# Performance work log

Hardware: AMD Instinct MI355X
Metric: run time of the kernel (lower is better)

The kernel has to match this reference:

```python
import jax, jax.numpy as jnp
import numpy as np

N, L, I, H, D = 8192, 8, 256, 512, 8
PER = N // D  # nodes per depth level; level 0 nodes are tree roots


def setup_inputs() -> dict:
    key = jax.random.key(0)
    ks = jax.random.split(key, 9)
    s = 0.05
    x_seq = jax.random.normal(ks[0], (N, L, I), jnp.float32)
    # GRU params (torch nn.GRU layout, gate order r,z,n), stored transposed [in, 3H]
    W_ih = jax.random.normal(ks[1], (I, 3 * H), jnp.float32) * s
    W_hh = jax.random.normal(ks[2], (H, 3 * H), jnp.float32) * s
    b_ih = jax.random.normal(ks[3], (3 * H,), jnp.float32) * s
    b_hh = jax.random.normal(ks[4], (3 * H,), jnp.float32) * s
    # Child-sum TreeLSTM params: x-projections for i,o,u,f and recurrent U's
    Wx = jax.random.normal(ks[5], (H, 4 * H), jnp.float32) * s
    bx = jax.random.normal(ks[6], (4 * H,), jnp.float32) * s
    U_iou = jax.random.normal(ks[7], (H, 3 * H), jnp.float32) * s
    U_f = jax.random.normal(ks[8], (H, H), jnp.float32) * s
    # Forest structure: D levels of PER nodes; node at level d>0 has a random
    # parent at level d-1; roots (level 0) point at themselves (contribution is
    # zero because their own state is still zero when level 0 is processed).
    rng = np.random.default_rng(0)
    depth = np.repeat(np.arange(D), PER).astype(np.int32)
    parent = np.arange(N, dtype=np.int32)
    for d in range(1, D):
        parent[d * PER:(d + 1) * PER] = rng.integers((d - 1) * PER, d * PER, PER)
    root_ids = np.arange(PER, dtype=np.int32)
    return {
        "x_seq": x_seq, "W_ih": W_ih, "W_hh": W_hh, "b_ih": b_ih, "b_hh": b_hh,
        "Wx": Wx, "bx": bx, "U_iou": U_iou, "U_f": U_f,
        "parent": jnp.asarray(parent), "depth": jnp.asarray(depth),
        "root_ids": jnp.asarray(root_ids), "n_levels": D,
    }


def reference(x_seq, W_ih, W_hh, b_ih, b_hh, Wx, bx, U_iou, U_f,
              parent, depth, root_ids, n_levels):
    n = x_seq.shape[0]
    h_dim = W_hh.shape[0]

    # --- GRU over each node's encoding sequence (all nodes batched) ---
    def gru_step(h, x_t):  # h: [N,H], x_t: [N,I]
        gi = x_t @ W_ih + b_ih
        gh = h @ W_hh + b_hh
        ir, iz, inn = jnp.split(gi, 3, axis=-1)
        hr, hz, hn = jnp.split(gh, 3, axis=-1)
        r = jax.nn.sigmoid(ir + hr)
        z = jax.nn.sigmoid(iz + hz)
        ng = jnp.tanh(inn + r * hn)
        return (1.0 - z) * ng + z * h, None

    h0 = jnp.zeros((n, h_dim), x_seq.dtype)
    enc, _ = jax.lax.scan(gru_step, h0, jnp.swapaxes(x_seq, 0, 1))  # [N,H]

    # --- Child-sum TreeLSTM, processed leaves -> roots by depth level ---
    xg = enc @ Wx + bx  # [N,4H]
    xi, xo, xu, xf = jnp.split(xg, 4, axis=-1)
    c = jnp.zeros((n, h_dim), x_seq.dtype)
    h = jnp.zeros((n, h_dim), x_seq.dtype)
    for level in range(n_levels - 1, -1, -1):
        h_sum = jax.ops.segment_sum(h, parent, num_segments=n)  # sum over children
        giou = h_sum @ U_iou
        i = jax.nn.sigmoid(xi + giou[:, :h_dim])
        o = jax.nn.sigmoid(xo + giou[:, h_dim:2 * h_dim])
        u = jnp.tanh(xu + giou[:, 2 * h_dim:])
        # per-child forget gate uses parent's x projection and child's h
        f = jax.nn.sigmoid(xf[parent] + h @ U_f)
        fc = jax.ops.segment_sum(f * c, parent, num_segments=n)
        c_new = i * u + fc
        mask = (depth == level)[:, None]
        c = jnp.where(mask, c_new, c)
        h = jnp.where(mask, o * jnp.tanh(c_new), h)

    # root states per tree, stacked as [2, n_trees, H] -> (c_root, h_root)
    return jnp.stack([c[root_ids], h[root_ids]])
```

## Files before the change

### kernel.cpp

```cpp
#include <hip/hip_runtime.h>
#include <math.h>

typedef short bf16x8 __attribute__((ext_vector_type(8)));
typedef float f32x4 __attribute__((ext_vector_type(4)));

__device__ __forceinline__ float sigf(float x) {
    return __builtin_amdgcn_rcpf(1.f + __expf(-x));
}
__device__ __forceinline__ float tanhf_fast(float x) {
    const float e = __expf(2.f * x);
    return 1.f - 2.f * __builtin_amdgcn_rcpf(e + 1.f);
}

__device__ __forceinline__ unsigned short f2bf(float f) {
    union { float f; unsigned u; } v; v.f = f;
    unsigned r = (v.u + 0x7FFFu + ((v.u >> 16) & 1u)) >> 16;
    return (unsigned short)r;
}
__device__ __forceinline__ float bf2f(unsigned short u) {
    union { unsigned u; float f; } v; v.u = ((unsigned)u) << 16; return v.f;
}

__device__ __forceinline__ void gload16(const unsigned short* g, unsigned short* l) {
    __builtin_amdgcn_global_load_lds(
        (const __attribute__((address_space(1))) void*)g,
        (__attribute__((address_space(3))) void*)l, 16, 0, 0);
}

__device__ __forceinline__ int swz(int slot, int row) {
    return (slot ^ ((row >> 1) & 3)) * 8;
}
__device__ __forceinline__ int tix(int ml, int jl) {
    return ((ml >> 4) * 2 + (jl >> 5)) * 512 + (ml & 15) * 32 + (jl & 31);
}

__global__ void cvt_f32_bf16(const float* __restrict__ src,
                             unsigned short* __restrict__ dst, int n)
{
    const int i = (blockIdx.x * blockDim.x + threadIdx.x) * 4;
    if (i >= n) return;
    const float4 v = *reinterpret_cast<const float4*>(src + i);
    ushort4 o;
    o.x = f2bf(v.x); o.y = f2bf(v.y); o.z = f2bf(v.z); o.w = f2bf(v.w);
    *reinterpret_cast<ushort4*>(dst + i) = o;
}

__global__ void transpose_cvt(const float* __restrict__ src,
                              unsigned short* __restrict__ dst,
                              int rows, int cols)
{
    __shared__ float tile[32][33];
    const int bc = blockIdx.x * 32, br = blockIdx.y * 32;
    const int tx = threadIdx.x, ty = threadIdx.y;
    #pragma unroll
    for (int i = 0; i < 32; i += 8)
        tile[ty + i][tx] = src[(size_t)(br + ty + i) * cols + bc + tx];
    __syncthreads();
    #pragma unroll
    for (int i = 0; i < 32; i += 8)
        dst[(size_t)(bc + ty + i) * rows + br + tx] = f2bf(tile[tx][ty + i]);
}

__global__ __launch_bounds__(256)
void gemm_bf16out(const unsigned short* __restrict__ A,
                  const unsigned short* __restrict__ BT,
                  const float* __restrict__ bias,
                  unsigned short* __restrict__ Cb, int M, int N, int K,
                  int ncols, int Mrows, int rstride, int tstride)
{
    const int nwg = (int)gridDim.x;
    const int l = ((int)blockIdx.x & 7) * (nwg >> 3) + ((int)blockIdx.x >> 3);
    const int m0 = (l / ncols) * 128, n0 = (l % ncols) * 128;
    const size_t abase = (size_t)(m0 % Mrows) * rstride
                       + (size_t)(m0 / Mrows) * tstride;
    const int tid = (int)threadIdx.x, lane = tid & 63, wid = tid >> 6;
    const int wm = wid >> 1, wn = wid & 1;
    const int fr = lane & 15, kg = lane >> 4;
    const int lrow = lane >> 2;
    const int scol = swz(lane & 3, lrow);

    __shared__ unsigned short smem[3 * 8192];

    f32x4 acc[4][4];
    #pragma unroll
    for (int i = 0; i < 4; ++i)
        #pragma unroll
        for (int j = 0; j < 4; ++j)
            acc[i][j] = (f32x4){0.f, 0.f, 0.f, 0.f};

    auto stage = [&](int buf, int kt) {
        const int k0 = kt * 32;
        unsigned short* base = &smem[buf * 8192];
        #pragma unroll
        for (int q = 0; q < 4; ++q) {
            const int c = wid * 4 + q;
            const unsigned short* g = (c < 8)
                ? A + abase + (size_t)(c * 16 + lrow) * rstride + k0 + scol
                : BT + (size_t)(n0 + (c - 8) * 16 + lrow) * K + k0 + scol;
            gload16(g, base + c * 512);
        }
    };

    const int nkt = K >> 5;
    stage(0, 0); stage(1, 1); stage(2, 2);
    int cur = 0;

    for (int kt = 0; kt < nkt; ++kt) {
        if (kt + 2 < nkt)      asm volatile("s_waitcnt vmcnt(8)" ::: "memory");
        else if (kt + 1 < nkt) asm volatile("s_waitcnt vmcnt(4)" ::: "memory");
        else                   asm volatile("s_waitcnt vmcnt(0)" ::: "memory");
        __builtin_amdgcn_s_barrier();

        const unsigned short* sb = &smem[cur * 8192];
        bf16x8 af[4], bf[4];
        #pragma unroll
        for (int mi = 0; mi < 4; ++mi) {
            const int row = wm * 64 + mi * 16 + fr;
            af[mi] = *reinterpret_cast<const bf16x8*>(&sb[row * 32 + swz(kg, row)]);
        }
        #pragma unroll
        for (int ni = 0; ni < 4; ++ni) {
            const int row = wn * 64 + ni * 16 + fr;
            bf[ni] = *reinterpret_cast<const bf16x8*>(&sb[4096 + row * 32 + swz(kg, row)]);
        }
        asm volatile("s_waitcnt lgkmcnt(0)" ::: "memory");
        __builtin_amdgcn_s_barrier();
        if (kt + 3 < nkt) stage(cur, kt + 3);

        __builtin_amdgcn_s_setprio(1);
        #pragma unroll
        for (int mi = 0; mi < 4; ++mi)
            #pragma unroll
            for (int ni = 0; ni < 4; ++ni)
                acc[mi][ni] = __builtin_amdgcn_mfma_f32_16x16x32_bf16(
                    af[mi], bf[ni], acc[mi][ni], 0, 0, 0);
        __builtin_amdgcn_s_setprio(0);
        cur = (cur == 2) ? 0 : cur + 1;
    }

    #pragma unroll
    for (int ni = 0; ni < 4; ++ni) {
        const int nl = wn * 64 + ni * 16 + fr;
        const float bv = bias[n0 + nl];
        #pragma unroll
        for (int mi = 0; mi < 4; ++mi)
            #pragma unroll
            for (int r = 0; r < 4; ++r) {
                const int ml = wm * 64 + mi * 16 + kg * 4 + r;
                smem[ml * 132 + nl] = f2bf(acc[mi][ni][r] + bv);
            }
    }
    __syncthreads();
    #pragma unroll
    for (int e = 0; e < 8; ++e) {
        const int id = tid + e * 256;
        const int row = id >> 4, cw = id & 15;
        const int4 v = *reinterpret_cast<const int4*>(&smem[row * 132 + cw * 8]);
        *reinterpret_cast<int4*>(&Cb[(size_t)(m0 + row) * N + n0 + cw * 8]) = v;
    }
}

__global__ void gru_step0(const unsigned short* __restrict__ gi,
                          unsigned short* __restrict__ hbo,
                          const float* __restrict__ b_hh)
{
    constexpr int H = 512, G3H = 1536;
    const int idx = blockIdx.x * blockDim.x + threadIdx.x;
    const int m = idx >> 6, jv = idx & 63;
    const size_t gb = (size_t)m * G3H + jv * 8;
    const bf16x8 gr8 = *reinterpret_cast<const bf16x8*>(gi + gb);
    const bf16x8 gz8 = *reinterpret_cast<const bf16x8*>(gi + gb + H);
    const bf16x8 gn8 = *reinterpret_cast<const bf16x8*>(gi + gb + 2 * H);
    bf16x8 o;
    #pragma unroll
    for (int k = 0; k < 8; ++k) {
        const int j = jv * 8 + k;
        const float r = sigf(bf2f((unsigned short)gr8[k]) + b_hh[j]);
        const float z = sigf(bf2f((unsigned short)gz8[k]) + b_hh[H + j]);
        const float n = tanhf_fast(bf2f((unsigned short)gn8[k]) + r * b_hh[2 * H + j]);
        o[k] = (short)f2bf((1.f - z) * n);
    }
    *reinterpret_cast<bf16x8*>(hbo + (size_t)m * H + jv * 8) = o;
}

__global__ __launch_bounds__(256, 3)
void gru_step(const unsigned short* __restrict__ giT,
              const unsigned short* __restrict__ hbi,
              unsigned short* __restrict__ hbo,
              const unsigned short* __restrict__ WhhT,
              const float* __restrict__ b_hh)
{
    constexpr int H = 512, G3H = 1536;
    const int m0 = blockIdx.x * 64, j0 = blockIdx.y * 64;
    const int tid = (int)threadIdx.x, lane = tid & 63, wid = tid >> 6;
    const int wm = wid >> 1, wn = wid & 1;
    const int fr = lane & 15, kg = lane >> 4;
    const int lrow = lane >> 2;
    const int scol = swz(lane & 3, lrow);
    const int ucol = (lane & 3) * 8;

    __shared__ unsigned short smem[3 * 8192];

    f32x4 ar[2][2], az[2][2], ah[2][2];
    #pragma unroll
    for (int i = 0; i < 2; ++i)
        #pragma unroll
        for (int j = 0; j < 2; ++j) {
            ar[i][j] = (f32x4){0.f, 0.f, 0.f, 0.f};
            az[i][j] = (f32x4){0.f, 0.f, 0.f, 0.f};
            ah[i][j] = (f32x4){0.f, 0.f, 0.f, 0.f};
        }

    constexpr int nkt = H / 32;

    auto stage = [&](int buf, int kt) {
        const int k0 = kt * 32;
        unsigned short* base = &smem[buf * 8192];
        #pragma unroll
        for (int q = 0; q < 4; ++q) {
            const int c = wid * 4 + q;
            if (c < 4) {
                const unsigned short* g =
                    hbi + (size_t)(m0 + c * 16 + lrow) * H + k0 + scol;
                gload16(g, base + c * 512);
            } else {
                const int gate = (c - 4) >> 2, rowg = (c - 4) & 3;
                const unsigned short* g =
                    WhhT + (size_t)(gate * H + j0 + rowg * 16 + lrow) * H + k0 + scol;
                gload16(g, base + c * 512);
            }
        }
    };
    auto stage_epi = [&](int ep) {
        unsigned short* base = &smem[(ep + 1) * 8192];
        #pragma unroll
        for (int q = 0; q < 4; ++q) {
            const int c = wid * 4 + q;
            const int part = c >> 3, cc = c & 7;
            const int rowg = cc >> 1, colg = cc & 1;
            const unsigned short* src;
            if (ep == 0)
                src = giT + (size_t)(m0 + rowg * 16 + lrow) * G3H
                          + part * H + j0 + colg * 32 + ucol;
            else if (part == 0)
                src = giT + (size_t)(m0 + rowg * 16 + lrow) * G3H
                          + 2 * H + j0 + colg * 32 + ucol;
            else
                src = hbi + (size_t)(m0 + rowg * 16 + lrow) * H
                          + j0 + colg * 32 + ucol;
            gload16(src, base + part * 4096 + cc * 512);
        }
    };

    stage(0, 0); stage(1, 1); stage(2, 2);
    int cur = 0;

    for (int kt = 0; kt < nkt; ++kt) {
        asm volatile("s_waitcnt vmcnt(8)" ::: "memory");
        __builtin_amdgcn_s_barrier();

        const unsigned short* sb = &smem[cur * 8192];
        bf16x8 af[2], bfr[2], bfz[2], bfn[2];
        #pragma unroll
        for (int mi = 0; mi < 2; ++mi) {
            const int row = wm * 32 + mi * 16 + fr;
            af[mi] = *reinterpret_cast<const bf16x8*>(&sb[row * 32 + swz(kg, row)]);
        }
        #pragma unroll
        for (int ni = 0; ni < 2; ++ni) {
            const int row = wn * 32 + ni * 16 + fr;
            const int sw = swz(kg, row);
            bfr[ni] = *reinterpret_cast<const bf16x8*>(&sb[2048 + (row) * 32 + sw]);
            bfz[ni] = *reinterpret_cast<const bf16x8*>(&sb[2048 + (64 + row) * 32 + sw]);
            bfn[ni] = *reinterpret_cast<const bf16x8*>(&sb[2048 + (128 + row) * 32 + sw]);
        }
        asm volatile("s_waitcnt lgkmcnt(0)" ::: "memory");
        __builtin_amdgcn_s_barrier();
        if (kt + 3 < nkt)       stage(cur, kt + 3);
        else if (kt == nkt - 3) stage_epi(0);
        else if (kt == nkt - 2) stage_epi(1);

        __builtin_amdgcn_s_setprio(1);
        #pragma unroll
        for (int mi = 0; mi < 2; ++mi)
            #pragma unroll
            for (int ni = 0; ni < 2; ++ni) {
                ar[mi][ni] = __builtin_amdgcn_mfma_f32_16x16x32_bf16(af[mi], bfr[ni], ar[mi][ni], 0, 0, 0);
                az[mi][ni] = __builtin_amdgcn_mfma_f32_16x16x32_bf16(af[mi], bfz[ni], az[mi][ni], 0, 0, 0);
                ah[mi][ni] = __builtin_amdgcn_mfma_f32_16x16x32_bf16(af[mi], bfn[ni], ah[mi][ni], 0, 0, 0);
            }
        __builtin_amdgcn_s_setprio(0);
        cur = (cur == 2) ? 0 : cur + 1;
    }

    asm volatile("s_waitcnt vmcnt(0)" ::: "memory");
    __builtin_amdgcn_s_barrier();

    unsigned short res[2][2][4];
    #pragma unroll
    for (int ni = 0; ni < 2; ++ni) {
        const int jl = wn * 32 + ni * 16 + fr;
        const int j = j0 + jl;
        const float bhr = b_hh[j], bhz = b_hh[H + j], bhn = b_hh[2 * H + j];
        #pragma unroll
        for (int mi = 0; mi < 2; ++mi) {
            #pragma unroll
            for (int r = 0; r < 4; ++r) {
                const int ml = wm * 32 + mi * 16 + kg * 4 + r;
                const int ix = tix(ml, jl);
                const float gr = bf2f(smem[8192 + ix]);
                const float gz = bf2f(smem[12288 + ix]);
                const float gn = bf2f(smem[16384 + ix]);
                const float hv = bf2f(smem[20480 + ix]);
                const float rg = sigf(ar[mi][ni][r] + gr + bhr);
                const float zg = sigf(az[mi][ni][r] + gz + bhz);
                const float ng = tanhf_fast(gn + rg * (ah[mi][ni][r] + bhn));
                res[ni][mi][r] = f2bf((1.f - zg) * ng + zg * hv);
            }
        }
    }

    #pragma unroll
    for (int ni = 0; ni < 2; ++ni) {
        const int jl = wn * 32 + ni * 16 + fr;
        #pragma unroll
        for (int mi = 0; mi < 2; ++mi)
            #pragma unroll
            for (int r = 0; r < 4; ++r) {
                const int ml = wm * 32 + mi * 16 + kg * 4 + r;
                smem[tix(ml, jl)] = res[ni][mi][r];
            }
    }
    __syncthreads();

    #pragma unroll
    for (int e = 0; e < 2; ++e) {
        const int id = tid + e * 256;
        const int ml = id >> 3, jw = id & 7;
        const int4 v = *reinterpret_cast<const int4*>(
            &smem[((ml >> 4) * 2 + (jw >> 2)) * 512 + (ml & 15) * 32 + (jw & 3) * 8]);
        *reinterpret_cast<int4*>(&hbo[(size_t)(m0 + ml) * H + j0 + jw * 8]) = v;
    }
}

__global__ __launch_bounds__(256, 4)
void tree_gemm(const unsigned short* __restrict__ hTb,
               const unsigned short* __restrict__ UcombT,
               const unsigned short* __restrict__ xgb,
               const float* __restrict__ cT,
               const int* __restrict__ parent,
               int cstart, int pstart,
               float* __restrict__ giou,
               float* __restrict__ fcs)
{
    constexpr int H = 512, N4H = 2048, G3H = 1536;
    const int nwg = (int)gridDim.x;
    const int l = ((int)blockIdx.x & 7) * (nwg >> 3) + ((int)blockIdx.x >> 3);
    const int m0 = (l >> 5) * 64, n0 = (l & 31) * 64;
    const int tid = (int)threadIdx.x, lane = tid & 63, wid = tid >> 6;
    const int wm = wid >> 1, wn = wid & 1;
    const int fr = lane & 15, kg = lane >> 4;
    const int lrow = lane >> 2;
    const int scol = swz(lane & 3, lrow);

    __shared__ unsigned short smem[4 * 4096];

    f32x4 acc[2][2];
    #pragma unroll
    for (int i = 0; i < 2; ++i)
        #pragma unroll
        for (int j = 0; j < 2; ++j)
            acc[i][j] = (f32x4){0.f, 0.f, 0.f, 0.f};

    auto stage = [&](int buf, int kt) {
        const int k0 = kt * 32;
        unsigned short* base = &smem[buf * 4096];
        #pragma unroll
        for (int q = 0; q < 2; ++q) {
            const int c = wid * 2 + q;
            const unsigned short* g = (c < 4)
                ? hTb + (size_t)(cstart + m0 + c * 16 + lrow) * H + k0 + scol
                : UcombT + (size_t)(n0 + (c - 4) * 16 + lrow) * H + k0 + scol;
            gload16(g, base + c * 512);
        }
    };

    constexpr int nkt = H / 32;
    stage(0, 0); stage(1, 1); stage(2, 2); stage(3, 3);
    int cur = 0;

    for (int kt = 0; kt < nkt; ++kt) {
        if (kt + 3 < nkt)      asm volatile("s_waitcnt vmcnt(6)" ::: "memory");
        else if (kt + 2 < nkt) asm volatile("s_waitcnt vmcnt(4)" ::: "memory");
        else if (kt + 1 < nkt) asm volatile("s_waitcnt vmcnt(2)" ::: "memory");
        else                   asm volatile("s_waitcnt vmcnt(0)" ::: "memory");
        __builtin_amdgcn_s_barrier();

        const unsigned short* sb = &smem[cur * 4096];
        bf16x8 af[2], bf[2];
        #pragma unroll
        for (int mi = 0; mi < 2; ++mi) {
            const int row = wm * 32 + mi * 16 + fr;
            af[mi] = *reinterpret_cast<const bf16x8*>(&sb[row * 32 + swz(kg, row)]);
        }
        #pragma unroll
        for (int ni = 0; ni < 2; ++ni) {
            const int row = wn * 32 + ni * 16 + fr;
            bf[ni] = *reinterpret_cast<const bf16x8*>(&sb[2048 + row * 32 + swz(kg, row)]);
        }
        asm volatile("s_waitcnt lgkmcnt(0)" ::: "memory");
        __builtin_amdgcn_s_barrier();
        if (kt + 4 < nkt) stage(cur, kt + 4);

        __builtin_amdgcn_s_setprio(1);
        #pragma unroll
        for (int mi = 0; mi < 2; ++mi)
            #pragma unroll
            for (int ni = 0; ni < 2; ++ni)
                acc[mi][ni] = __builtin_amdgcn_mfma_f32_16x16x32_bf16(
                    af[mi], bf[ni], acc[mi][ni], 0, 0, 0);
        __builtin_amdgcn_s_setprio(0);
        cur = (cur == 3) ? 0 : cur + 1;
    }

    if (n0 < G3H) {
        #pragma unroll
        for (int mi = 0; mi < 2; ++mi)
            #pragma unroll
            for (int r = 0; r < 4; ++r) {
                const int m = m0 + wm * 32 + mi * 16 + kg * 4 + r;
                const int p = parent[cstart + m] - pstart;
                #pragma unroll
                for (int ni = 0; ni < 2; ++ni) {
                    const int n = n0 + wn * 32 + ni * 16 + fr;
                    atomicAdd(&giou[(size_t)p * G3H + n], acc[mi][ni][r]);
                }
            }
    } else {
        #pragma unroll
        for (int mi = 0; mi < 2; ++mi)
            #pragma unroll
            for (int r = 0; r < 4; ++r) {
                const int m = m0 + wm * 32 + mi * 16 + kg * 4 + r;
                const int child = cstart + m;
                const int p = parent[child];
                #pragma unroll
                for (int ni = 0; ni < 2; ++ni) {
                    const int jf = n0 + wn * 32 + ni * 16 + fr - G3H;
                    const float f = sigf(acc[mi][ni][r] +
                                         bf2f(xgb[(size_t)p * N4H + G3H + jf]));
                    atomicAdd(&fcs[(size_t)(p - pstart) * H + jf],
                              f * cT[(size_t)child * H + jf]);
                }
            }
    }
}

__global__ void level_update(const unsigned short* __restrict__ xgb,
                             float* __restrict__ giou,
                             float* __restrict__ fcs,
                             float* __restrict__ cT, float* __restrict__ hT,
                             unsigned short* __restrict__ hb, int pstart,
                             float* __restrict__ outp, int PH)
{
    constexpr int H = 512, N4H = 2048, G3H = 1536;
    const int idx = blockIdx.x * blockDim.x + threadIdx.x;
    const int pi = idx >> 9, j = idx & (H - 1);
    const int p = pstart + pi;
    const size_t xb4 = (size_t)p * N4H;
    const size_t gb = (size_t)pi * G3H;
    const float ig = sigf(bf2f(xgb[xb4 + j]) + giou[gb + j]);
    const float og = sigf(bf2f(xgb[xb4 + H + j]) + giou[gb + H + j]);
    const float ug = tanhf_fast(bf2f(xgb[xb4 + 2 * H + j]) + giou[gb + 2 * H + j]);
    const float cn = ig * ug + fcs[idx];
    const float hn = og * tanhf_fast(cn);
    if (outp) {
        outp[idx] = cn;
        outp[(size_t)PH + idx] = hn;
    } else {
        const size_t off = (size_t)p * H + j;
        cT[off] = cn;
        hT[off] = hn;
        hb[off] = f2bf(hn);
        giou[gb + j] = 0.f;
        giou[gb + H + j] = 0.f;
        giou[gb + 2 * H + j] = 0.f;
        fcs[idx] = 0.f;
    }
}

extern "C" void kernel_launch(void* const* d_in, const int* in_sizes, int n_in,
                              void* d_out, int out_size, void* d_ws, size_t ws_size,
                              hipStream_t stream)
{
    const float* x_seq = (const float*)d_in[0];
    const float* W_ih  = (const float*)d_in[1];
    const float* W_hh  = (const float*)d_in[2];
    const float* b_ih  = (const float*)d_in[3];
    const float* b_hh  = (const float*)d_in[4];
    const float* Wx    = (const float*)d_in[5];
    const float* bx    = (const float*)d_in[6];
    const float* U_iou = (const float*)d_in[7];
    const float* U_f   = (const float*)d_in[8];
    const int* parent  = (const int*)d_in[9];

    const int threeH = in_sizes[3];
    const int H   = threeH / 3;
    const int I   = in_sizes[1] / threeH;
    const int N   = in_sizes[9];
    const int L   = in_sizes[0] / (N * I);
    const int PER = in_sizes[11];
    const int D   = N / PER;

    const size_t NH = (size_t)N * H;
    const size_t PH = (size_t)PER * H;
    const size_t NG = (size_t)N * threeH;

    char* p = (char*)d_ws;
    const size_t xb_sz  = (size_t)N * L * I * 2;
    const size_t xgb_sz = (size_t)N * 4 * H * 2;
    const size_t zone_sz = xb_sz > xgb_sz ? xb_sz : xgb_sz;
    unsigned short* xb  = (unsigned short*)p;
    unsigned short* xgb = (unsigned short*)p;    p += zone_sz;
    unsigned short* gi  = (unsigned short*)p;    p += (size_t)N * L * threeH * 2;
    unsigned short* hb0 = (unsigned short*)p;    p += NH * 2;
    unsigned short* hb1 = (unsigned short*)p;    p += NH * 2;
    unsigned short* WihT = (unsigned short*)p;   p += (size_t)threeH * I * 2;
    unsigned short* WhhT = (unsigned short*)p;   p += (size_t)threeH * H * 2;
    unsigned short* WxT  = (unsigned short*)p;   p += (size_t)4 * H * H * 2;
    unsigned short* UcombT = (unsigned short*)p; p += (size_t)4 * H * H * 2;
    if ((size_t)(p - (char*)d_ws) > ws_size) return;
    float* cT   = (float*)gi;
    float* hT   = cT + NH;
    float* giou = hT + NH;
    float* fcs  = giou + PH * 3;

    {
        const int n = N * L * I;
        cvt_f32_bf16<<<(n / 4 + 255) / 256, 256, 0, stream>>>(x_seq, xb, n);
        dim3 blk(32, 8);
        transpose_cvt<<<dim3(threeH / 32, I / 32), blk, 0, stream>>>(W_ih, WihT, I, threeH);
        transpose_cvt<<<dim3(threeH / 32, H / 32), blk, 0, stream>>>(W_hh, WhhT, H, threeH);
        transpose_cvt<<<dim3(4 * H / 32, H / 32), blk, 0, stream>>>(Wx, WxT, H, 4 * H);
        transpose_cvt<<<dim3(threeH / 32, H / 32), blk, 0, stream>>>(U_iou, UcombT, H, threeH);
        transpose_cvt<<<dim3(H / 32, H / 32), blk, 0, stream>>>(
            U_f, UcombT + (size_t)threeH * H, H, H);
    }

    gemm_bf16out<<<(N * L / 128) * (threeH / 128), 256, 0, stream>>>(
        xb, WihT, b_ih, gi, N * L, threeH, I, threeH / 128,
        N, L * I, I);

    gru_step0<<<(int)(NH / 8 / 256), 256, 0, stream>>>(gi, hb1, b_hh);
    {
        dim3 grid(N / 64, H / 64);
        for (int t = 1; t < L; ++t) {
            const unsigned short* hin = (t & 1) ? hb1 : hb0;
            unsigned short* hout = (t & 1) ? hb0 : hb1;
            gru_step<<<grid, 256, 0, stream>>>(gi + (size_t)t * NG, hin, hout,
                                               WhhT, b_hh);
        }
    }

    gemm_bf16out<<<(N / 128) * (4 * H / 128), 256, 0, stream>>>(
        hb0, WxT, bx, xgb, N, 4 * H, H, 4 * H / 128,
        N, H, 0);

    hipMemsetAsync(giou, 0, PH * 4 * 4, stream);
    unsigned short* hTb = hb1;
    const int pw_blocks = (int)(PH / 256);

    for (int lvl = D - 1; lvl >= 0; --lvl) {
        const int pstart = lvl * PER;
        const int cstart = (lvl + 1) * PER;

        if (lvl < D - 1)
            tree_gemm<<<(PER / 64) * (4 * H / 64), 256, 0, stream>>>(
                hTb, UcombT, xgb, cT, parent, cstart, pstart, giou, fcs);

        level_update<<<pw_blocks, 256, 0, stream>>>(
            xgb, giou, fcs, cT, hT, hTb, pstart,
            (lvl == 0) ? (float*)d_out : nullptr, (int)PH);
    }
}
```

Measured before the change: 471.8 us.

## Double-buffer GRU step for higher occupancy and merge setup launches

The GRU recurrent step kernel drops from triple to double buffering in LDS and raises launch bounds from 3 to 4 blocks per CU, aiming for higher occupancy. The epilogue operands now reuse the two buffers, which requires an extra barrier. The five weight-transpose launches are folded into one kernel that picks its source by block index. The memset of the tree accumulators is replaced by a priming flag on the first level_update, which skips reading them and always zeroes them. The cost is a shallower prefetch pipeline in the GRU step, which may expose more memory latency.

```diff
diff --git a/kernel.cpp b/kernel.cpp
--- a/kernel.cpp
+++ b/kernel.cpp
@@ -45,12 +45,28 @@
     *reinterpret_cast<ushort4*>(dst + i) = o;
 }
 
-__global__ void transpose_cvt(const float* __restrict__ src,
-                              unsigned short* __restrict__ dst,
-                              int rows, int cols)
-{
+__global__ void transpose_all(const float* __restrict__ W_ih,
+                              const float* __restrict__ W_hh,
+                              const float* __restrict__ Wx,
+                              const float* __restrict__ U_iou,
+                              const float* __restrict__ U_f,
+                              unsigned short* __restrict__ WihT,
+                              unsigned short* __restrict__ WhhT,
+                              unsigned short* __restrict__ WxT,
+                              unsigned short* __restrict__ UcombT,
+                              int threeH, int I, int H,
+                              int n1, int n2, int n3, int n4)
+{
+    int b = (int)blockIdx.x;
+    const float* src; unsigned short* dst; int rows, cols;
+    if (b < n1)      { src = W_ih;  dst = WihT;   rows = I; cols = threeH; }
+    else if (b < n2) { src = W_hh;  dst = WhhT;   rows = H; cols = threeH; b -= n1; }
+    else if (b < n3) { src = Wx;    dst = WxT;    rows = H; cols = 4 * H;  b -= n2; }
+    else if (b < n4) { src = U_iou; dst = UcombT; rows = H; cols = threeH; b -= n3; }
+    else { src = U_f; dst = UcombT + (size_t)threeH * H; rows = H; cols = H; b -= n4; }
+    const int ncx = cols / 32;
+    const int bc = (b % ncx) * 32, br = (b / ncx) * 32;
     __shared__ float tile[32][33];
-    const int bc = blockIdx.x * 32, br = blockIdx.y * 32;
     const int tx = threadIdx.x, ty = threadIdx.y;
     #pragma unroll
     for (int i = 0; i < 32; i += 8)
@@ -183,7 +199,7 @@
     *reinterpret_cast<bf16x8*>(hbo + (size_t)m * H + jv * 8) = o;
 }
 
-__global__ __launch_bounds__(256, 3)
+__global__ __launch_bounds__(256, 4)
 void gru_step(const unsigned short* __restrict__ giT,
               const unsigned short* __restrict__ hbi,
               unsigned short* __restrict__ hbo,
@@ -199,7 +215,7 @@
     const int scol = swz(lane & 3, lrow);
     const int ucol = (lane & 3) * 8;
 
-    __shared__ unsigned short smem[3 * 8192];
+    __shared__ unsigned short smem[2 * 8192];
 
     f32x4 ar[2][2], az[2][2], ah[2][2];
     #pragma unroll
@@ -224,7 +240,7 @@
                     hbi + (size_t)(m0 + c * 16 + lrow) * H + k0 + scol;
                 gload16(g, base + c * 512);
             } else {
-                const int gate = (c - 4) >> 2, rowg = (c - 4) & 3;
+                const int bc = c - 4, gate = bc >> 2, rowg = bc & 3;
                 const unsigned short* g =
                     WhhT + (size_t)(gate * H + j0 + rowg * 16 + lrow) * H + k0 + scol;
                 gload16(g, base + c * 512);
@@ -232,7 +248,7 @@
         }
     };
     auto stage_epi = [&](int ep) {
-        unsigned short* base = &smem[(ep + 1) * 8192];
+        unsigned short* base = &smem[ep * 8192];
         #pragma unroll
         for (int q = 0; q < 4; ++q) {
             const int c = wid * 4 + q;
@@ -252,14 +268,13 @@
         }
     };
 
-    stage(0, 0); stage(1, 1); stage(2, 2);
-    int cur = 0;
+    stage(0, 0); stage(1, 1);
 
     for (int kt = 0; kt < nkt; ++kt) {
-        asm volatile("s_waitcnt vmcnt(8)" ::: "memory");
+        asm volatile("s_waitcnt vmcnt(4)" ::: "memory");
         __builtin_amdgcn_s_barrier();
 
-        const unsigned short* sb = &smem[cur * 8192];
+        const unsigned short* sb = &smem[(kt & 1) * 8192];
         bf16x8 af[2], bfr[2], bfz[2], bfn[2];
         #pragma unroll
         for (int mi = 0; mi < 2; ++mi) {
@@ -276,9 +291,9 @@
         }
         asm volatile("s_waitcnt lgkmcnt(0)" ::: "memory");
         __builtin_amdgcn_s_barrier();
-        if (kt + 3 < nkt)       stage(cur, kt + 3);
-        else if (kt == nkt - 3) stage_epi(0);
-        else if (kt == nkt - 2) stage_epi(1);
+        if (kt + 2 < nkt)       stage(kt & 1, kt + 2);
+        else if (kt == nkt - 2) stage_epi(0);
+        else                    stage_epi(1);
 
         __builtin_amdgcn_s_setprio(1);
         #pragma unroll
@@ -290,7 +305,6 @@
                 ah[mi][ni] = __builtin_amdgcn_mfma_f32_16x16x32_bf16(af[mi], bfn[ni], ah[mi][ni], 0, 0, 0);
             }
         __builtin_amdgcn_s_setprio(0);
-        cur = (cur == 2) ? 0 : cur + 1;
     }
 
     asm volatile("s_waitcnt vmcnt(0)" ::: "memory");
@@ -308,10 +322,10 @@
             for (int r = 0; r < 4; ++r) {
                 const int ml = wm * 32 + mi * 16 + kg * 4 + r;
                 const int ix = tix(ml, jl);
-                const float gr = bf2f(smem[8192 + ix]);
-                const float gz = bf2f(smem[12288 + ix]);
-                const float gn = bf2f(smem[16384 + ix]);
-                const float hv = bf2f(smem[20480 + ix]);
+                const float gr = bf2f(smem[ix]);
+                const float gz = bf2f(smem[4096 + ix]);
+                const float gn = bf2f(smem[8192 + ix]);
+                const float hv = bf2f(smem[12288 + ix]);
                 const float rg = sigf(ar[mi][ni][r] + gr + bhr);
                 const float zg = sigf(az[mi][ni][r] + gz + bhz);
                 const float ng = tanhf_fast(gn + rg * (ah[mi][ni][r] + bhn));
@@ -319,6 +333,7 @@
             }
         }
     }
+    __syncthreads();
 
     #pragma unroll
     for (int ni = 0; ni < 2; ++ni) {
@@ -461,7 +476,7 @@
                              float* __restrict__ fcs,
                              float* __restrict__ cT, float* __restrict__ hT,
                              unsigned short* __restrict__ hb, int pstart,
-                             float* __restrict__ outp, int PH)
+                             float* __restrict__ outp, int PH, int prime)
 {
     constexpr int H = 512, N4H = 2048, G3H = 1536;
     const int idx = blockIdx.x * blockDim.x + threadIdx.x;
@@ -469,10 +484,15 @@
     const int p = pstart + pi;
     const size_t xb4 = (size_t)p * N4H;
     const size_t gb = (size_t)pi * G3H;
-    const float ig = sigf(bf2f(xgb[xb4 + j]) + giou[gb + j]);
-    const float og = sigf(bf2f(xgb[xb4 + H + j]) + giou[gb + H + j]);
-    const float ug = tanhf_fast(bf2f(xgb[xb4 + 2 * H + j]) + giou[gb + 2 * H + j]);
-    const float cn = ig * ug + fcs[idx];
+    float gv0 = 0.f, gv1 = 0.f, gv2 = 0.f, fv = 0.f;
+    if (!prime) {
+        gv0 = giou[gb + j]; gv1 = giou[gb + H + j];
+        gv2 = giou[gb + 2 * H + j]; fv = fcs[idx];
+    }
+    const float ig = sigf(bf2f(xgb[xb4 + j]) + gv0);
+    const float og = sigf(bf2f(xgb[xb4 + H + j]) + gv1);
+    const float ug = tanhf_fast(bf2f(xgb[xb4 + 2 * H + j]) + gv2);
+    const float cn = ig * ug + fv;
     const float hn = og * tanhf_fast(cn);
     if (outp) {
         outp[idx] = cn;
@@ -482,11 +502,11 @@
         cT[off] = cn;
         hT[off] = hn;
         hb[off] = f2bf(hn);
-        giou[gb + j] = 0.f;
-        giou[gb + H + j] = 0.f;
-        giou[gb + 2 * H + j] = 0.f;
-        fcs[idx] = 0.f;
-    }
+    }
+    giou[gb + j] = 0.f;
+    giou[gb + H + j] = 0.f;
+    giou[gb + 2 * H + j] = 0.f;
+    fcs[idx] = 0.f;
 }
 
 extern "C" void kernel_launch(void* const* d_in, const int* in_sizes, int n_in,
@@ -538,13 +558,14 @@
     {
         const int n = N * L * I;
         cvt_f32_bf16<<<(n / 4 + 255) / 256, 256, 0, stream>>>(x_seq, xb, n);
-        dim3 blk(32, 8);
-        transpose_cvt<<<dim3(threeH / 32, I / 32), blk, 0, stream>>>(W_ih, WihT, I, threeH);
-        transpose_cvt<<<dim3(threeH / 32, H / 32), blk, 0, stream>>>(W_hh, WhhT, H, threeH);
-        transpose_cvt<<<dim3(4 * H / 32, H / 32), blk, 0, stream>>>(Wx, WxT, H, 4 * H);
-        transpose_cvt<<<dim3(threeH / 32, H / 32), blk, 0, stream>>>(U_iou, UcombT, H, threeH);
-        transpose_cvt<<<dim3(H / 32, H / 32), blk, 0, stream>>>(
-            U_f, UcombT + (size_t)threeH * H, H, H);
+        const int n1 = (threeH / 32) * (I / 32);
+        const int n2 = n1 + (threeH / 32) * (H / 32);
+        const int n3 = n2 + (4 * H / 32) * (H / 32);
+        const int n4 = n3 + (threeH / 32) * (H / 32);
+        const int n5 = n4 + (H / 32) * (H / 32);
+        transpose_all<<<n5, dim3(32, 8), 0, stream>>>(
+            W_ih, W_hh, Wx, U_iou, U_f, WihT, WhhT, WxT, UcombT,
+            threeH, I, H, n1, n2, n3, n4);
     }
 
     gemm_bf16out<<<(N * L / 128) * (threeH / 128), 256, 0, stream>>>(
@@ -566,7 +587,6 @@
         hb0, WxT, bx, xgb, N, 4 * H, H, 4 * H / 128,
         N, H, 0);
 
-    hipMemsetAsync(giou, 0, PH * 4 * 4, stream);
     unsigned short* hTb = hb1;
     const int pw_blocks = (int)(PH / 256);
 
@@ -580,6 +600,7 @@
 
         level_update<<<pw_blocks, 256, 0, stream>>>(
             xgb, giou, fcs, cT, hT, hTb, pstart,
-            (lvl == 0) ? (float*)d_out : nullptr, (int)PH);
-    }
-}
+            (lvl == 0) ? (float*)d_out : nullptr, (int)PH,
+            (lvl == D - 1) ? 1 : 0);
+    }
+}
```

After: 462.7 us. No clear change (-1.9%).
